# Optimization experiments

Hardware: AMD Instinct MI355X
Metric: run time of the kernel (lower is better)

## Reference

```python
import jax, jax.numpy as jnp
import numpy as np

N, K = 16384, 16
SIZE, DIST = 256, 64
HEADS, ATTN = 8, 32
HIDDEN = 512
HA = HEADS * ATTN  # 256
EDGE = SIZE + DIST  # key/value input size per edge


def setup_inputs() -> dict:
    key = jax.random.key(0)
    ks = jax.random.split(key, 16)
    s = lambda k, fi, fo: jax.random.normal(k, (fi, fo), jnp.float32) / np.sqrt(fi)
    return {
        "features": jax.random.normal(ks[0], (N, SIZE), jnp.float32),
        "distances": jax.random.normal(ks[1], (N, K, DIST), jnp.float32),
        "structure": jax.random.randint(ks[2], (N, K), 0, N, jnp.int32),
        # local MLP: size -> hidden -> hidden -> size (depth=3 linears)
        "W0": s(ks[3], SIZE, HIDDEN), "b0": jnp.zeros((HIDDEN,), jnp.float32),
        "W1": s(ks[4], HIDDEN, HIDDEN), "b1": jnp.zeros((HIDDEN,), jnp.float32),
        "W2": s(ks[5], HIDDEN, SIZE), "b2": jnp.zeros((SIZE,), jnp.float32),
        # neighbour dot multi-head attention
        "Wq": s(ks[6], SIZE, HA), "bq": jnp.zeros((HA,), jnp.float32),
        "Wk": s(ks[7], EDGE, HA), "bk": jnp.zeros((HA,), jnp.float32),
        "Wv": s(ks[8], EDGE, HA), "bv": jnp.zeros((HA,), jnp.float32),
        "Wo": s(ks[9], HA, SIZE), "bo": jnp.zeros((SIZE,), jnp.float32),
    }


def reference(features, distances, structure,
              W0, b0, W1, b1, W2, b2,
              Wq, bq, Wk, bk, Wv, bv, Wo, bo):
    # batch_norm=False -> bn layers are identity; activation = relu
    inputs = jax.nn.relu(features)                      # [N, size]
    # local MLP (ReLU between layers), then outer activation
    h = jax.nn.relu(inputs @ W0 + b0)
    h = jax.nn.relu(h @ W1 + b1)
    local = jax.nn.relu(h @ W2 + b2)                    # [N, size]
    # edge structure: gather neighbour features, concat distance features
    neigh = local[structure]                            # [N, K, size]
    edge = jnp.concatenate([neigh, distances], axis=-1) # [N, K, size+dist]
    # neighbour-restricted multi-head dot attention
    q = (features @ Wq + bq).reshape(N, HEADS, ATTN)    # [N, H, A]
    k = (edge @ Wk + bk).reshape(N, K, HEADS, ATTN)     # [N, K, H, A]
    v = (edge @ Wv + bv).reshape(N, K, HEADS, ATTN)
    scale = jnp.float32(1.0 / np.sqrt(ATTN))
    scores = jnp.einsum('nha,nkha->nhk', q, k) * scale  # [N, H, K]
    attn = jax.nn.softmax(scores, axis=-1)
    o = jnp.einsum('nhk,nkha->nha', attn, v).reshape(N, HA)
    out = o @ Wo + bo                                   # [N, size]
    return features + out
```

## Files before the change

kernel.cpp:

```cpp
#include <hip/hip_runtime.h>
#include <hip/hip_bf16.h>

#define NN 16384
#define SIZE 256
#define DISTD 64
#define KNBR 16
#define HEADS 8
#define HIDDEN 512
#define HA 256
#define SCALE 0.17677669529663687f

typedef __bf16 bf16;
typedef bf16 bf16x2 __attribute__((ext_vector_type(2)));
typedef bf16 bf16x4 __attribute__((ext_vector_type(4)));
typedef bf16 bf16x8 __attribute__((ext_vector_type(8)));
typedef float f32x4 __attribute__((ext_vector_type(4)));

__device__ __forceinline__ void gload16(const void* g, void* l) {
    __builtin_amdgcn_global_load_lds(
        (const __attribute__((address_space(1))) unsigned int*)g,
        (__attribute__((address_space(3))) unsigned int*)l, 16, 0, 0);
}

template<bool BIAS, bool RELU_OUT, bool RESID, typename OutT, int TN>
__global__ __launch_bounds__(256) void gemm128(
    const bf16* __restrict__ A, const bf16* __restrict__ BT,
    const float* __restrict__ bias, const float* __restrict__ resid,
    OutT* __restrict__ C, int M, int N, int K)
{
    constexpr int NF = TN / 32;
    __shared__ alignas(16) bf16 As[2][128][32];
    __shared__ alignas(16) bf16 Bs[2][TN][32];

    const int t = threadIdx.x;
    const int w = t >> 6, l = t & 63;
    const int bm = blockIdx.y * 128, bn = blockIdx.x * TN;
    const int wr = (w >> 1) * 64, wc = (w & 1) * (TN / 2);

    f32x4 acc[4][NF] = {};

    const bf16* ag = A  + (size_t)(bm + (t >> 2)) * K + (t & 3) * 8;
    const bf16* bg = BT + (size_t)(bn + (t >> 2)) * K + (t & 3) * 8;

    const int nt = K >> 5;
    {
        bf16* asl = &As[0][w << 4][0];
        bf16* bsl = &Bs[0][w << 4][0];
        gload16(ag, asl);
        gload16(ag + (size_t)64 * K, (char*)asl + 4096);
        gload16(bg, bsl);
        if constexpr (TN == 128)
            gload16(bg + (size_t)64 * K, (char*)bsl + 4096);
    }
    __syncthreads();

    for (int tt = 0; tt < nt; ++tt) {
        const int cur = tt & 1;
        if (tt + 1 < nt) {
            const int k0 = (tt + 1) << 5;
            bf16* asl = &As[cur ^ 1][w << 4][0];
            bf16* bsl = &Bs[cur ^ 1][w << 4][0];
            gload16(ag + k0, asl);
            gload16(ag + k0 + (size_t)64 * K, (char*)asl + 4096);
            gload16(bg + k0, bsl);
            if constexpr (TN == 128)
                gload16(bg + k0 + (size_t)64 * K, (char*)bsl + 4096);
        }
        bf16x8 af[4], bfr[NF];
        #pragma unroll
        for (int m = 0; m < 4; ++m)
            af[m] = *(const bf16x8*)&As[cur][wr + m * 16 + (l & 15)][(l >> 4) * 8];
        #pragma unroll
        for (int n2 = 0; n2 < NF; ++n2)
            bfr[n2] = *(const bf16x8*)&Bs[cur][wc + n2 * 16 + (l & 15)][(l >> 4) * 8];
        #pragma unroll
        for (int m = 0; m < 4; ++m)
            #pragma unroll
            for (int n2 = 0; n2 < NF; ++n2)
                acc[m][n2] = __builtin_amdgcn_mfma_f32_16x16x32_bf16(
                    af[m], bfr[n2], acc[m][n2], 0, 0, 0);
        __syncthreads();
    }

    #pragma unroll
    for (int m = 0; m < 4; ++m) {
        const int row = bm + wr + m * 16 + ((l >> 4) << 2);
        #pragma unroll
        for (int n2 = 0; n2 < NF; ++n2) {
            const int col = bn + wc + n2 * 16 + (l & 15);
            #pragma unroll
            for (int i = 0; i < 4; ++i) {
                float v = acc[m][n2][i];
                if (BIAS) v += bias[col];
                if (RESID) v += resid[(size_t)(row + i) * N + col];
                if (RELU_OUT) v = fmaxf(v, 0.f);
                C[(size_t)(row + i) * N + col] = (OutT)v;
            }
        }
    }
}

__global__ __launch_bounds__(256) void g1qcat_kernel(
    const bf16* __restrict__ fbf, const bf16* __restrict__ frbf,
    const bf16* __restrict__ W0T, const float* __restrict__ b0,
    const bf16* __restrict__ WqcatT, const float* __restrict__ bqcat,
    bf16* __restrict__ H0, bf16* __restrict__ qcat)
{
    __shared__ alignas(16) bf16 As[2][128][32];
    __shared__ alignas(16) bf16 Bs[2][128][32];

    const int bx = blockIdx.x, by = blockIdx.y;
    const bool isG1 = bx < 4;
    const int cx = bx - 4;
    const bf16* A  = isG1 ? frbf : fbf;
    const bf16* BT = isG1 ? (W0T + (size_t)bx * 128 * 256)
                          : (WqcatT + (size_t)cx * 128 * 256);
    const float* bias = isG1 ? (b0 + bx * 128) : (bqcat + cx * 128);
    const int K = 256;

    const int t = threadIdx.x;
    const int w = t >> 6, l = t & 63;
    const int bm = by * 128;
    const int wr = (w >> 1) * 64, wc = (w & 1) * 64;

    f32x4 acc[4][4] = {};

    const bf16* ag = A  + (size_t)(bm + (t >> 2)) * K + (t & 3) * 8;
    const bf16* bg = BT + (size_t)(t >> 2) * K + (t & 3) * 8;

    {
        bf16* asl = &As[0][w << 4][0];
        bf16* bsl = &Bs[0][w << 4][0];
        gload16(ag, asl);
        gload16(ag + (size_t)64 * K, (char*)asl + 4096);
        gload16(bg, bsl);
        gload16(bg + (size_t)64 * K, (char*)bsl + 4096);
    }
    __syncthreads();

    for (int tt = 0; tt < 8; ++tt) {
        const int cur = tt & 1;
        if (tt + 1 < 8) {
            const int k0 = (tt + 1) << 5;
            bf16* asl = &As[cur ^ 1][w << 4][0];
            bf16* bsl = &Bs[cur ^ 1][w << 4][0];
            gload16(ag + k0, asl);
            gload16(ag + k0 + (size_t)64 * K, (char*)asl + 4096);
            gload16(bg + k0, bsl);
            gload16(bg + k0 + (size_t)64 * K, (char*)bsl + 4096);
        }
        bf16x8 af[4], bfr[4];
        #pragma unroll
        for (int m = 0; m < 4; ++m)
            af[m] = *(const bf16x8*)&As[cur][wr + m * 16 + (l & 15)][(l >> 4) * 8];
        #pragma unroll
        for (int n2 = 0; n2 < 4; ++n2)
            bfr[n2] = *(const bf16x8*)&Bs[cur][wc + n2 * 16 + (l & 15)][(l >> 4) * 8];
        #pragma unroll
        for (int m = 0; m < 4; ++m)
            #pragma unroll
            for (int n2 = 0; n2 < 4; ++n2)
                acc[m][n2] = __builtin_amdgcn_mfma_f32_16x16x32_bf16(
                    af[m], bfr[n2], acc[m][n2], 0, 0, 0);
        __syncthreads();
    }

    #pragma unroll
    for (int m = 0; m < 4; ++m) {
        const int lrow = wr + m * 16 + ((l >> 4) << 2);
        #pragma unroll
        for (int n2 = 0; n2 < 4; ++n2) {
            const int lcol = wc + n2 * 16 + (l & 15);
            #pragma unroll
            for (int i = 0; i < 4; ++i) {
                float v = acc[m][n2][i] + bias[lcol];
                const size_t row = bm + lrow + i;
                if (isG1) {
                    H0[row * 512 + bx * 128 + lcol] = (bf16)fmaxf(v, 0.f);
                } else {
                    qcat[row * 768 + cx * 128 + lcol] = (bf16)v;
                }
            }
        }
    }
}

__global__ __launch_bounds__(256) void prep_all(
    const float* __restrict__ features,
    const float* __restrict__ W0, const float* __restrict__ W1,
    const float* __restrict__ W2, const float* __restrict__ Wq,
    const float* __restrict__ bq, const float* __restrict__ Wk,
    const float* __restrict__ Wv, const float* __restrict__ Wo,
    const float* __restrict__ bo, const float* __restrict__ bv,
    bf16* __restrict__ fbf, bf16* __restrict__ frbf,
    bf16* __restrict__ W0T, bf16* __restrict__ W1T, bf16* __restrict__ W2T,
    bf16* __restrict__ WkvT, bf16* __restrict__ WqcatT, bf16* __restrict__ WstackT,
    float* __restrict__ bqcat, float* __restrict__ biaso)
{
    if (blockIdx.x < 4096) {
        int id = blockIdx.x * 256 + threadIdx.x;
        float4 v = ((const float4*)features)[id];
        bf16x4 a, r;
        a[0] = (bf16)v.x; a[1] = (bf16)v.y; a[2] = (bf16)v.z; a[3] = (bf16)v.w;
        r[0] = (bf16)fmaxf(v.x, 0.f); r[1] = (bf16)fmaxf(v.y, 0.f);
        r[2] = (bf16)fmaxf(v.z, 0.f); r[3] = (bf16)fmaxf(v.w, 0.f);
        ((bf16x4*)fbf)[id] = a; ((bf16x4*)frbf)[id] = r;
        return;
    }
    long id = (blockIdx.x - 4096) * 256L + threadIdx.x;
    if (id < 131072) {
        int n = id >> 8, k = id & 255;
        W0T[id] = (bf16)W0[(long)k * 512 + n]; return;
    }
    id -= 131072;
    if (id < 262144) {
        int n = id >> 9, k = id & 511;
        W1T[id] = (bf16)W1[(long)k * 512 + n]; return;
    }
    id -= 262144;
    if (id < 131072) {
        int n = id >> 9, k = id & 511;
        W2T[id] = (bf16)W2[(long)k * 256 + n]; return;
    }
    id -= 131072;
    if (id < 131072) {
        int n = id >> 8, k = id & 255;
        WkvT[id] = (bf16)(n < 256 ? Wk[(long)k * 256 + n] : Wv[(long)k * 256 + (n - 256)]);
        return;
    }
    id -= 131072;
    if (id < 196608) {
        int col = id >> 8, c = id & 255;
        float s;
        if (col < 256) s = Wq[(long)c * 256 + col];
        else {
            int hd = col - 256, h = hd >> 6, d = hd & 63;
            s = 0.f;
            #pragma unroll
            for (int a = 0; a < 32; ++a)
                s += Wq[(long)c * 256 + h * 32 + a] * Wk[(long)(256 + d) * 256 + h * 32 + a];
        }
        WqcatT[id] = (bf16)(s * SCALE); return;
    }
    id -= 196608;
    if (id < 196608) {
        int col = (int)(id / 768), r = (int)(id % 768);
        float s;
        if (r < 256) s = Wo[(long)r * 256 + col];
        else {
            int hd = r - 256, h = hd >> 6, d = hd & 63;
            s = 0.f;
            #pragma unroll
            for (int a = 0; a < 32; ++a)
                s += Wv[(long)(256 + d) * 256 + h * 32 + a] * Wo[(long)(h * 32 + a) * 256 + col];
        }
        WstackT[id] = (bf16)s; return;
    }
    id -= 196608;
    if (id < 768) {
        float s;
        if (id < 256) s = bq[id];
        else {
            int hd = (int)id - 256, h = hd >> 6, d = hd & 63;
            s = 0.f;
            #pragma unroll
            for (int a = 0; a < 32; ++a)
                s += bq[h * 32 + a] * Wk[(long)(256 + d) * 256 + h * 32 + a];
        }
        bqcat[id] = s * SCALE; return;
    }
    id -= 768;
    if (id < 256) {
        float s = bo[id];
        for (int u = 0; u < 256; ++u) s += bv[u] * Wo[(long)u * 256 + id];
        biaso[id] = s;
    }
}

__global__ __launch_bounds__(256) void attn_kernel(
    const bf16* __restrict__ qcat,
    const bf16* __restrict__ localKV,
    const float* __restrict__ dist,
    const int*  __restrict__ structure,
    bf16* __restrict__ concat)
{
    const int n = blockIdx.x;
    const int t = threadIdx.x;
    const int h = t >> 5, j = (t >> 1) & 15, part = t & 1;

    __shared__ float dist_s[16][65];
    __shared__ bf16  V_s[16][264];
    __shared__ float attn_s[8][16];
    __shared__ int   s_s[16];

    {
        const float* dp = dist + (long)n * (KNBR * DISTD);
        #pragma unroll
        for (int i = 0; i < 4; ++i) {
            int e = i * 256 + t;
            dist_s[e >> 6][e & 63] = dp[e];
        }
    }
    if (t < 16) s_s[t] = structure[(long)n * KNBR + t];
    __syncthreads();

    #pragma unroll
    for (int pass = 0; pass < 2; ++pass) {
        int idx = pass * 256 + t;
        int row = idx >> 5, chunk = idx & 31;
        bf16x8 v = *(const bf16x8*)(localKV + (long)s_s[row] * 512 + 256 + chunk * 8);
        *(bf16x8*)&V_s[row][chunk * 8] = v;
    }

    const bf16* qp_q = qcat + (long)n * 768 + h * 32 + part * 16;
    bf16x8 qa = *(const bf16x8*)qp_q;
    bf16x8 qb = *(const bf16x8*)(qp_q + 8);
    const bf16* qp_p = qcat + (long)n * 768 + 256 + h * 64 + part * 32;
    bf16x8 p0 = *(const bf16x8*)qp_p;
    bf16x8 p1 = *(const bf16x8*)(qp_p + 8);
    bf16x8 p2 = *(const bf16x8*)(qp_p + 16);
    bf16x8 p3 = *(const bf16x8*)(qp_p + 24);
    const bf16* kp = localKV + (long)s_s[j] * 512 + h * 32 + part * 16;
    bf16x8 ka = *(const bf16x8*)kp;
    bf16x8 kb = *(const bf16x8*)(kp + 8);

    float sc = 0.f;
    #pragma unroll
    for (int i = 0; i < 8; ++i)
        sc += (float)qa[i] * (float)ka[i] + (float)qb[i] * (float)kb[i];

    const int dbase = part * 32;
    #pragma unroll
    for (int i = 0; i < 8; ++i) sc += dist_s[j][dbase + i]      * (float)p0[i];
    #pragma unroll
    for (int i = 0; i < 8; ++i) sc += dist_s[j][dbase + 8 + i]  * (float)p1[i];
    #pragma unroll
    for (int i = 0; i < 8; ++i) sc += dist_s[j][dbase + 16 + i] * (float)p2[i];
    #pragma unroll
    for (int i = 0; i < 8; ++i) sc += dist_s[j][dbase + 24 + i] * (float)p3[i];

    sc += __shfl_xor(sc, 1);
    float m = sc;
    m = fmaxf(m, __shfl_xor(m, 2));
    m = fmaxf(m, __shfl_xor(m, 4));
    m = fmaxf(m, __shfl_xor(m, 8));
    m = fmaxf(m, __shfl_xor(m, 16));
    float e = __expf(sc - m);
    float sum = e;
    sum += __shfl_xor(sum, 2);
    sum += __shfl_xor(sum, 4);
    sum += __shfl_xor(sum, 8);
    sum += __shfl_xor(sum, 16);
    float attn = e / sum;
    if (!part) attn_s[h][j] = attn;
    __syncthreads();

    float acc = 0.f;
    #pragma unroll
    for (int j2 = 0; j2 < 16; ++j2)
        acc += attn_s[h][j2] * (float)V_s[j2][t];
    concat[(long)n * 768 + t] = (bf16)acc;

    #pragma unroll
    for (int rep = 0; rep < 2; ++rep) {
        int idx = rep * 256 + t;
        int h3 = idx >> 6, d3 = idx & 63;
        float s2 = 0.f;
        #pragma unroll
        for (int j2 = 0; j2 < 16; ++j2)
            s2 += attn_s[h3][j2] * dist_s[j2][d3];
        concat[(long)n * 768 + 256 + idx] = (bf16)s2;
    }
}

extern "C" void kernel_launch(void* const* d_in, const int* in_sizes, int n_in,
                              void* d_out, int out_size, void* d_ws, size_t ws_size,
                              hipStream_t stream)
{
    const float* features = (const float*)d_in[0];
    const float* dist     = (const float*)d_in[1];
    const int*   structure= (const int*)d_in[2];
    const float* W0 = (const float*)d_in[3];
    const float* b0 = (const float*)d_in[4];
    const float* W1 = (const float*)d_in[5];
    const float* b1 = (const float*)d_in[6];
    const float* W2 = (const float*)d_in[7];
    const float* b2 = (const float*)d_in[8];
    const float* Wq = (const float*)d_in[9];
    const float* bq = (const float*)d_in[10];
    const float* Wk = (const float*)d_in[11];
    const float* Wv = (const float*)d_in[13];
    const float* bv = (const float*)d_in[14];
    const float* Wo = (const float*)d_in[15];
    const float* bo = (const float*)d_in[16];
    float* out = (float*)d_out;

    const size_t MB = 1u << 20;
    char* w = (char*)d_ws;
    bf16*  fbf     = (bf16*)(w + 0 * MB);
    bf16*  local_b = (bf16*)(w + 0 * MB);
    bf16*  frbf    = (bf16*)(w + 8 * MB);
    bf16*  localKV = (bf16*)(w + 8 * MB);
    bf16*  H0      = (bf16*)(w + 16 * MB);
    bf16*  qcat    = (bf16*)(w + 32 * MB);
    bf16*  H1      = (bf16*)(w + 56 * MB);
    bf16*  concat  = (bf16*)(w + 56 * MB);
    char*  wb      = w + 80 * MB;
    bf16*  W0T     = (bf16*)(wb + 0);
    bf16*  W1T     = (bf16*)(wb + 262144);
    bf16*  W2T     = (bf16*)(wb + 786432);
    bf16*  WkvT    = (bf16*)(wb + 1048576);
    bf16*  WqcatT  = (bf16*)(wb + 1310720);
    bf16*  WstackT = (bf16*)(wb + 1703936);
    float* bqcat   = (float*)(wb + 2097152);
    float* biaso   = (float*)(wb + 2100224);

    dim3 blk(256);

    prep_all<<<dim3(8196), blk, 0, stream>>>(
        features, W0, W1, W2, Wq, bq, Wk, Wv, Wo, bo, bv,
        fbf, frbf, W0T, W1T, W2T, WkvT, WqcatT, WstackT, bqcat, biaso);

    g1qcat_kernel<<<dim3(10, 128), blk, 0, stream>>>(
        fbf, frbf, W0T, b0, WqcatT, bqcat, H0, qcat);

    gemm128<true,  true,  false, bf16, 64><<<dim3(8, 128), blk, 0, stream>>>(
        H0, W1T, b1, nullptr, H1, NN, 512, 512);
    gemm128<true,  true,  false, bf16, 64><<<dim3(4, 128), blk, 0, stream>>>(
        H1, W2T, b2, nullptr, local_b, NN, 256, 512);
    gemm128<false, false, false, bf16, 64><<<dim3(8, 128), blk, 0, stream>>>(
        local_b, WkvT, nullptr, nullptr, localKV, NN, 512, 256);

    attn_kernel<<<dim3(NN), blk, 0, stream>>>(
        qcat, localKV, dist, structure, concat);

    gemm128<true,  false, true,  float, 64><<<dim3(4, 128), blk, 0, stream>>>(
        concat, WstackT, biaso, features, out, NN, 256, 768);
}
```

Baseline: 178.1 us.

## Enlarge GEMM tiles to 128x128 with BK=64 and vectorize attention output

The generic GEMM is changed from a 128xTN tile with BK=32 to a fixed 128x128 tile that stages two 32-wide K sub-slices per pipeline step (BK=64), halving grid width and barrier count per K. This is meant to raise arithmetic intensity per block and cut synchronisation overhead, at the cost of double the LDS and more accumulator registers, which lowers occupancy and wave count. In the attention kernel the weighted V and distance reductions are split across thread halves with vectorized bf16x2/f32x4 loads and stores. dist_s padding is changed to 68 so rows are 16-byte aligned.

Measured after the change: 162.1 us. 1.1x faster.

```diff
diff --git a/kernel.cpp b/kernel.cpp
--- a/kernel.cpp
+++ b/kernel.cpp
@@ -22,63 +22,62 @@
         (__attribute__((address_space(3))) unsigned int*)l, 16, 0, 0);
 }
 
-template<bool BIAS, bool RELU_OUT, bool RESID, typename OutT, int TN>
+template<bool BIAS, bool RELU_OUT, bool RESID, typename OutT, int SUBS>
 __global__ __launch_bounds__(256) void gemm128(
     const bf16* __restrict__ A, const bf16* __restrict__ BT,
     const float* __restrict__ bias, const float* __restrict__ resid,
     OutT* __restrict__ C, int M, int N, int K)
 {
-    constexpr int NF = TN / 32;
-    __shared__ alignas(16) bf16 As[2][128][32];
-    __shared__ alignas(16) bf16 Bs[2][TN][32];
+    __shared__ alignas(16) bf16 As[2][SUBS][128][32];
+    __shared__ alignas(16) bf16 Bs[2][SUBS][128][32];
 
     const int t = threadIdx.x;
     const int w = t >> 6, l = t & 63;
-    const int bm = blockIdx.y * 128, bn = blockIdx.x * TN;
-    const int wr = (w >> 1) * 64, wc = (w & 1) * (TN / 2);
-
-    f32x4 acc[4][NF] = {};
+    const int bm = blockIdx.y * 128, bn = blockIdx.x * 128;
+    const int wr = (w >> 1) * 64, wc = (w & 1) * 64;
+    const int BK = 32 * SUBS;
+
+    f32x4 acc[4][4] = {};
 
     const bf16* ag = A  + (size_t)(bm + (t >> 2)) * K + (t & 3) * 8;
     const bf16* bg = BT + (size_t)(bn + (t >> 2)) * K + (t & 3) * 8;
 
-    const int nt = K >> 5;
-    {
-        bf16* asl = &As[0][w << 4][0];
-        bf16* bsl = &Bs[0][w << 4][0];
-        gload16(ag, asl);
-        gload16(ag + (size_t)64 * K, (char*)asl + 4096);
-        gload16(bg, bsl);
-        if constexpr (TN == 128)
-            gload16(bg + (size_t)64 * K, (char*)bsl + 4096);
-    }
+    auto STAGE = [&](int buf, int k0) {
+        #pragma unroll
+        for (int s = 0; s < SUBS; ++s) {
+            bf16* asl = &As[buf][s][w << 4][0];
+            bf16* bsl = &Bs[buf][s][w << 4][0];
+            gload16(ag + k0 + s * 32, asl);
+            gload16(ag + k0 + s * 32 + (size_t)64 * K, (char*)asl + 4096);
+            gload16(bg + k0 + s * 32, bsl);
+            gload16(bg + k0 + s * 32 + (size_t)64 * K, (char*)bsl + 4096);
+        }
+    };
+
+    const int nt = K / BK;
+    STAGE(0, 0);
     __syncthreads();
 
     for (int tt = 0; tt < nt; ++tt) {
         const int cur = tt & 1;
-        if (tt + 1 < nt) {
-            const int k0 = (tt + 1) << 5;
-            bf16* asl = &As[cur ^ 1][w << 4][0];
-            bf16* bsl = &Bs[cur ^ 1][w << 4][0];
-            gload16(ag + k0, asl);
-            gload16(ag + k0 + (size_t)64 * K, (char*)asl + 4096);
-            gload16(bg + k0, bsl);
-            if constexpr (TN == 128)
-                gload16(bg + k0 + (size_t)64 * K, (char*)bsl + 4096);
-        }
-        bf16x8 af[4], bfr[NF];
-        #pragma unroll
-        for (int m = 0; m < 4; ++m)
-            af[m] = *(const bf16x8*)&As[cur][wr + m * 16 + (l & 15)][(l >> 4) * 8];
-        #pragma unroll
-        for (int n2 = 0; n2 < NF; ++n2)
-            bfr[n2] = *(const bf16x8*)&Bs[cur][wc + n2 * 16 + (l & 15)][(l >> 4) * 8];
-        #pragma unroll
-        for (int m = 0; m < 4; ++m)
-            #pragma unroll
-            for (int n2 = 0; n2 < NF; ++n2)
-                acc[m][n2] = __builtin_amdgcn_mfma_f32_16x16x32_bf16(
-                    af[m], bfr[n2], acc[m][n2], 0, 0, 0);
+        if (tt + 1 < nt) STAGE(cur ^ 1, (tt + 1) * BK);
+
+        #pragma unroll
+        for (int s = 0; s < SUBS; ++s) {
+            bf16x8 af[4], bfr[4];
+            #pragma unroll
+            for (int m = 0; m < 4; ++m)
+                af[m] = *(const bf16x8*)&As[cur][s][wr + m * 16 + (l & 15)][(l >> 4) * 8];
+            #pragma unroll
+            for (int n2 = 0; n2 < 4; ++n2)
+                bfr[n2] = *(const bf16x8*)&Bs[cur][s][wc + n2 * 16 + (l & 15)][(l >> 4) * 8];
+            #pragma unroll
+            for (int m = 0; m < 4; ++m)
+                #pragma unroll
+                for (int n2 = 0; n2 < 4; ++n2)
+                    acc[m][n2] = __builtin_amdgcn_mfma_f32_16x16x32_bf16(
+                        af[m], bfr[n2], acc[m][n2], 0, 0, 0);
+        }
         __syncthreads();
     }
 
@@ -86,7 +85,7 @@
     for (int m = 0; m < 4; ++m) {
         const int row = bm + wr + m * 16 + ((l >> 4) << 2);
         #pragma unroll
-        for (int n2 = 0; n2 < NF; ++n2) {
+        for (int n2 = 0; n2 < 4; ++n2) {
             const int col = bn + wc + n2 * 16 + (l & 15);
             #pragma unroll
             for (int i = 0; i < 4; ++i) {
@@ -288,7 +287,7 @@
     const int t = threadIdx.x;
     const int h = t >> 5, j = (t >> 1) & 15, part = t & 1;
 
-    __shared__ float dist_s[16][65];
+    __shared__ float dist_s[16][68];
     __shared__ bf16  V_s[16][264];
     __shared__ float attn_s[8][16];
     __shared__ int   s_s[16];
@@ -355,21 +354,34 @@
     if (!part) attn_s[h][j] = attn;
     __syncthreads();
 
-    float acc = 0.f;
-    #pragma unroll
-    for (int j2 = 0; j2 < 16; ++j2)
-        acc += attn_s[h][j2] * (float)V_s[j2][t];
-    concat[(long)n * 768 + t] = (bf16)acc;
-
-    #pragma unroll
-    for (int rep = 0; rep < 2; ++rep) {
-        int idx = rep * 256 + t;
-        int h3 = idx >> 6, d3 = idx & 63;
-        float s2 = 0.f;
-        #pragma unroll
-        for (int j2 = 0; j2 < 16; ++j2)
-            s2 += attn_s[h3][j2] * dist_s[j2][d3];
-        concat[(long)n * 768 + 256 + idx] = (bf16)s2;
+    if (t < 128) {
+        const int c0 = t * 2;
+        const int hh = t >> 4;
+        float a0 = 0.f, a1 = 0.f;
+        #pragma unroll
+        for (int j2 = 0; j2 < 16; ++j2) {
+            float wgt = attn_s[hh][j2];
+            bf16x2 pv = *(const bf16x2*)&V_s[j2][c0];
+            a0 += wgt * (float)pv[0];
+            a1 += wgt * (float)pv[1];
+        }
+        bf16x2 o2; o2[0] = (bf16)a0; o2[1] = (bf16)a1;
+        *(bf16x2*)&concat[(long)n * 768 + c0] = o2;
+    } else {
+        const int u = t - 128;
+        const int base = u * 4;
+        const int h3 = u >> 4, d3 = (u & 15) * 4;
+        f32x4 acc4 = {};
+        #pragma unroll
+        for (int j2 = 0; j2 < 16; ++j2) {
+            float wgt = attn_s[h3][j2];
+            const f32x4 dv = *(const f32x4*)&dist_s[j2][d3];
+            acc4 += wgt * dv;
+        }
+        bf16x4 o4;
+        #pragma unroll
+        for (int i = 0; i < 4; ++i) o4[i] = (bf16)acc4[i];
+        *(bf16x4*)&concat[(long)n * 768 + 256 + base] = o4;
     }
 }
 
@@ -424,16 +436,16 @@
     g1qcat_kernel<<<dim3(10, 128), blk, 0, stream>>>(
         fbf, frbf, W0T, b0, WqcatT, bqcat, H0, qcat);
 
-    gemm128<true,  true,  false, bf16, 64><<<dim3(8, 128), blk, 0, stream>>>(
+    gemm128<true,  true,  false, bf16, 2><<<dim3(4, 128), blk, 0, stream>>>(
         H0, W1T, b1, nullptr, H1, NN, 512, 512);
-    gemm128<true,  true,  false, bf16, 64><<<dim3(4, 128), blk, 0, stream>>>(
+    gemm128<true,  true,  false, bf16, 2><<<dim3(2, 128), blk, 0, stream>>>(
         H1, W2T, b2, nullptr, local_b, NN, 256, 512);
-    gemm128<false, false, false, bf16, 64><<<dim3(8, 128), blk, 0, stream>>>(
+    gemm128<false, false, false, bf16, 2><<<dim3(4, 128), blk, 0, stream>>>(
         local_b, WkvT, nullptr, nullptr, localKV, NN, 512, 256);
 
     attn_kernel<<<dim3(NN), blk, 0, stream>>>(
         qcat, localKV, dist, structure, concat);
 
-    gemm128<true,  false, true,  float, 64><<<dim3(4, 128), blk, 0, stream>>>(
+    gemm128<true,  false, true,  float, 2><<<dim3(2, 128), blk, 0, stream>>>(
         concat, WstackT, biaso, features, out, NN, 256, 768);
 }
```
